# Kernel optimization log

Measured on AMD Instinct MI355X. Metric: run time of the kernel, lower is better.

The kernel has to match this reference:

```python
import jax, jax.numpy as jnp
import numpy as np

EPS = 1e-8

def setup_inputs() -> dict:
    key = jax.random.key(0)
    ks = jax.random.split(key, 7)
    B, S, H, NH, V = 4, 2048, 1024, 8, 2048
    sc = 1.0 / np.sqrt(H)
    return {
        "hidden": jax.random.normal(ks[0], (B, S, H), jnp.float32),
        "prior_w": jax.random.normal(ks[1], (H, NH), jnp.float32) * sc,
        "prior_b": jnp.zeros((NH,), jnp.float32),
        "latent_w": jax.random.normal(ks[2], (H, NH * H), jnp.float32) * sc,
        "latent_b": jnp.zeros((NH * H,), jnp.float32),
        "output_w": jax.random.normal(ks[3], (H, V), jnp.float32) * sc,
        "output_b": jnp.zeros((V,), jnp.float32),
    }

def reference(hidden, prior_w, prior_b, latent_w, latent_b, output_w, output_b):
    B, S, H = hidden.shape
    NH = prior_w.shape[1]
    # prior: sigmoid then renormalize over heads
    prior = jax.nn.sigmoid(hidden @ prior_w + prior_b)              # [B,S,NH]
    prior = prior / (prior.sum(-1, keepdims=True) + EPS)
    # latent: linear -> [B,S,NH,H] -> tanh
    latent = jnp.tanh((hidden @ latent_w + latent_b).reshape(B, S, NH, H))
    # per-head softmax over vocab, weighted sum over heads
    logits = jnp.einsum('bsnh,hv->bsnv', latent, output_w) + output_b
    probs = jax.nn.softmax(logits, axis=-1)                          # [B,S,NH,V]
    return jnp.einsum('bsn,bsnv->bsv', prior, probs)
```

## Files before the change

### kernel.cpp

```cpp
#include <hip/hip_runtime.h>
#include <hip/hip_bf16.h>
#include <stdint.h>

typedef _Float16 f16;
typedef _Float16 f16x8 __attribute__((ext_vector_type(8)));
typedef _Float16 f16x4 __attribute__((ext_vector_type(4)));
typedef float f32x4 __attribute__((ext_vector_type(4)));
typedef float f32x16 __attribute__((ext_vector_type(16)));

#define T_TOK 8192
#define H_DIM 1024
#define NHEAD 8
#define V_DIM 2048

__device__ __forceinline__ void gload16(const void* g, void* l) {
  __builtin_amdgcn_global_load_lds(
      (const __attribute__((address_space(1))) void*)(uintptr_t)g,
      (__attribute__((address_space(3))) void*)(unsigned)(uintptr_t)l,
      16, 0, 0);
}

__device__ __forceinline__ float fast_tanh(float x) {
  float xc = fminf(fmaxf(x, -12.f), 12.f);
  float e = __expf(2.f * xc);
  return (e - 1.f) / (e + 1.f);
}

__device__ __forceinline__ void stage_half(const f16* __restrict__ gRowBase,
                                           char* ldsHalf, int tid, int sl8,
                                           int Kd) {
  const int srow = tid >> 3;
  char* wuni = ldsHalf + ((tid >> 6) << 10);
  gload16(gRowBase + (size_t)srow * Kd + sl8, wuni);
  gload16(gRowBase + (size_t)(srow + 64) * Kd + sl8, wuni + 8192);
}

template <int TANH>
__global__ __launch_bounds__(512, 2) void k_gemm(const f16* __restrict__ A,
                                                 const f16* __restrict__ Bt,
                                                 const float* __restrict__ bias,
                                                 f16* __restrict__ C,
                                                 int M, int N, int K) {
  __shared__ __align__(16) f16 sA[2][16384];
  __shared__ __align__(16) f16 sB[2][16384];
  const int tid = threadIdx.x;
  const int lane = tid & 63;
  const int wid = tid >> 6;
  const int wr = wid >> 2, wc = wid & 3;
  const int gx = gridDim.x;
  const int id = blockIdx.y * gx + blockIdx.x;
  const int cpx = (gx * gridDim.y) >> 3;
  const int sw = (id & 7) * cpx + (id >> 3);
  const int m0 = (sw / gx) * 256, n0 = (sw % gx) * 256;
  const int NT = K >> 6;
  const int sl8 = ((tid & 7) ^ ((tid >> 3) & 7)) << 3;
  const int rr31 = lane & 31;
  const int hi = lane >> 5;
  const int l7 = lane & 7;

  const f16* Ag = A + (size_t)m0 * K;
  const f16* Bg = Bt + (size_t)n0 * K;
  char* sAb = (char*)&sA[0][0];
  char* sBb = (char*)&sB[0][0];

  stage_half(Ag, sAb, tid, sl8, K);
  stage_half(Ag + (size_t)128 * K, sAb + 16384, tid, sl8, K);
  stage_half(Bg, sBb, tid, sl8, K);
  stage_half(Bg + (size_t)128 * K, sBb + 16384, tid, sl8, K);
  stage_half(Bg + 64, sBb + 32768, tid, sl8, K);
  stage_half(Bg + (size_t)128 * K + 64, sBb + 32768 + 16384, tid, sl8, K);
  asm volatile("s_waitcnt vmcnt(4)" ::: "memory");
  __builtin_amdgcn_s_barrier();
  __builtin_amdgcn_sched_barrier(0);

  f32x16 acc[4][2] = {};
  f16x8 af0[4], af1[4], bf[2][4];

#define LDA_SET(dst, base, q)                                                  \
  {                                                                            \
    _Pragma("unroll") for (int mi = 0; mi < 4; ++mi) {                         \
      dst[mi] = *(const f16x8*)((base) + wr * 16384 + mi * 4096 + rr31 * 128 + \
                                (((2 * (q) + hi) ^ l7) << 4));                 \
    }                                                                          \
  }
#define LDB(base)                                                              \
  {                                                                            \
    _Pragma("unroll") for (int n = 0; n < 2; ++n) {                            \
      _Pragma("unroll") for (int ks = 0; ks < 4; ++ks) {                       \
        bf[n][ks] = *(const f16x8*)((base) + wc * 8192 + n * 4096 +            \
                                    rr31 * 128 + (((2 * ks + hi) ^ l7) << 4)); \
      }                                                                        \
    }                                                                          \
  }
#define MFMA8(ks, S)                                                           \
  {                                                                            \
    __builtin_amdgcn_s_setprio(1);                                             \
    _Pragma("unroll") for (int mi = 0; mi < 4; ++mi) {                         \
      _Pragma("unroll") for (int n = 0; n < 2; ++n) {                          \
        acc[mi][n] = __builtin_amdgcn_mfma_f32_32x32x16_f16(                   \
            S[mi], bf[n][ks], acc[mi][n], 0, 0, 0);                            \
      }                                                                        \
    }                                                                          \
    __builtin_amdgcn_s_setprio(0);                                             \
  }

  LDA_SET(af0, sAb, 0);

#define HALF(tt, bc)                                                           \
  {                                                                            \
    const char* cA = sAb + (bc)*32768;                                         \
    const char* cB = sBb + (bc)*32768;                                         \
    char* nA = sAb + ((bc) ^ 1) * 32768;                                       \
    char* nB = sBb + (bc)*32768;                                               \
    const int ktA = ((tt) + 1) << 6, ktB = ((tt) + 2) << 6;                    \
    const bool doA = (tt) + 1 < NT, doB = (tt) + 2 < NT;                       \
                                                                      \
    if (doA) stage_half(Ag + ktA, nA, tid, sl8, K);                            \
    LDB(cB);                                                                   \
    LDA_SET(af1, cA, 1);                                                       \
    __builtin_amdgcn_sched_barrier(0);                                         \
    MFMA8(0, af0);                                                             \
    __builtin_amdgcn_s_barrier();                                              \
                                                                      \
    if (doA) stage_half(Ag + (size_t)128 * K + ktA, nA + 16384, tid, sl8, K);  \
    LDA_SET(af0, cA, 2);                                                       \
    __builtin_amdgcn_sched_barrier(0);                                         \
    MFMA8(1, af1);                                                             \
    __builtin_amdgcn_s_barrier();                                              \
                                                                      \
    if (doB) stage_half(Bg + ktB, nB, tid, sl8, K);                            \
    LDA_SET(af1, cA, 3);                                                       \
    __builtin_amdgcn_sched_barrier(0);                                         \
    MFMA8(2, af0);                                                             \
    __builtin_amdgcn_s_barrier();                                              \
                  \
    if (doB) stage_half(Bg + (size_t)128 * K + ktB, nB + 16384, tid, sl8, K);  \
    if (doB) {                                                                 \
      asm volatile("s_waitcnt vmcnt(4)" ::: "memory");                         \
    } else {                                                                   \
      asm volatile("s_waitcnt vmcnt(0)" ::: "memory");                         \
    }                                                                          \
    __builtin_amdgcn_s_barrier();                                              \
    __builtin_amdgcn_sched_barrier(0);                                         \
    if (doA) LDA_SET(af0, sAb + ((bc) ^ 1) * 32768, 0);                        \
    __builtin_amdgcn_sched_barrier(0);                                         \
    MFMA8(3, af1);                                                             \
  }

#pragma unroll 1
  for (int T = 0; T < NT; T += 2) {
    HALF(T, 0);
    HALF(T + 1, 1);
  }
#undef HALF
#undef LDA_SET
#undef LDB
#undef MFMA8

  const int ccol0 = n0 + wc * 64 + rr31;
  float bv[2];
#pragma unroll
  for (int n = 0; n < 2; ++n) bv[n] = bias[ccol0 + n * 32];
#pragma unroll
  for (int mi = 0; mi < 4; ++mi) {
#pragma unroll
    for (int rq = 0; rq < 4; ++rq) {
#pragma unroll
      for (int r2 = 0; r2 < 4; ++r2) {
        const int row = m0 + wr * 128 + mi * 32 + r2 + 8 * rq + 4 * hi;
        f16* Crow = C + (size_t)row * N;
#pragma unroll
        for (int n = 0; n < 2; ++n) {
          float v = acc[mi][n][rq * 4 + r2] + bv[n];
          if (TANH) v = fast_tanh(v);
          Crow[ccol0 + n * 32] = (f16)v;
        }
      }
    }
  }
}

__global__ __launch_bounds__(256) void k_convert(const float* __restrict__ in,
                                                 f16* __restrict__ out, int n4) {
  int i = blockIdx.x * blockDim.x + threadIdx.x;
  if (i >= n4) return;
  const float4 v = ((const float4*)in)[i];
  f16x4 o;
  o[0] = (f16)v.x; o[1] = (f16)v.y; o[2] = (f16)v.z; o[3] = (f16)v.w;
  ((f16x4*)out)[i] = o;
}

__global__ void k_transpose(const float* __restrict__ in, f16* __restrict__ out,
                            int R, int C) {
  __shared__ f16 tile[32][33];
  int c0 = blockIdx.x * 32, r0 = blockIdx.y * 32;
  for (int j = threadIdx.y; j < 32; j += 8)
    tile[j][threadIdx.x] = (f16)in[(size_t)(r0 + j) * C + (c0 + threadIdx.x)];
  __syncthreads();
  for (int j = threadIdx.y; j < 32; j += 8)
    out[(size_t)(c0 + j) * R + (r0 + threadIdx.x)] = tile[threadIdx.x][j];
}

__global__ __launch_bounds__(256) void k_prior(const float* __restrict__ hidden,
                                               const float* __restrict__ pw,
                                               const float* __restrict__ pb,
                                               float* __restrict__ prior) {
  const int wid = threadIdx.x >> 6, lane = threadIdx.x & 63;
  const int t = blockIdx.x * 4 + wid;
  float acc[NHEAD] = {0.f, 0.f, 0.f, 0.f, 0.f, 0.f, 0.f, 0.f};
  const float* hrow = hidden + (size_t)t * H_DIM;
  for (int k = lane; k < H_DIM; k += 64) {
    float x = hrow[k];
    const float* wr = pw + k * NHEAD;
#pragma unroll
    for (int h = 0; h < NHEAD; ++h) acc[h] += x * wr[h];
  }
#pragma unroll
  for (int h = 0; h < NHEAD; ++h) {
#pragma unroll
    for (int off = 32; off >= 1; off >>= 1) acc[h] += __shfl_xor(acc[h], off);
  }
  if (lane == 0) {
    float p[NHEAD], s = 0.f;
#pragma unroll
    for (int h = 0; h < NHEAD; ++h) {
      p[h] = 1.f / (1.f + __expf(-(acc[h] + pb[h])));
      s += p[h];
    }
    float inv = 1.f / (s + 1e-8f);
#pragma unroll
    for (int h = 0; h < NHEAD; ++h) prior[t * NHEAD + h] = p[h] * inv;
  }
}

__global__ __launch_bounds__(256) void k_softmax(const f16* __restrict__ logits,
                                                 const float* __restrict__ prior,
                                                 float* __restrict__ out) {
  __shared__ float red[4];
  const int t = blockIdx.x;
  const int tid = threadIdx.x, lane = tid & 63, wid = tid >> 6;
  float oa[8] = {0.f, 0.f, 0.f, 0.f, 0.f, 0.f, 0.f, 0.f};
  const int v0 = tid * 8;
#pragma unroll 1
  for (int h = 0; h < NHEAD; ++h) {
    f16x8 x = *(const f16x8*)(logits + ((size_t)t * NHEAD + h) * V_DIM + v0);
    float xv[8], mx = -1e30f;
#pragma unroll
    for (int j = 0; j < 8; j++) { xv[j] = (float)x[j]; mx = fmaxf(mx, xv[j]); }
#pragma unroll
    for (int off = 32; off >= 1; off >>= 1) mx = fmaxf(mx, __shfl_xor(mx, off));
    if (lane == 0) red[wid] = mx;
    __syncthreads();
    mx = fmaxf(fmaxf(red[0], red[1]), fmaxf(red[2], red[3]));
    __syncthreads();
    float e[8], s = 0.f;
#pragma unroll
    for (int j = 0; j < 8; j++) { e[j] = __expf(xv[j] - mx); s += e[j]; }
#pragma unroll
    for (int off = 32; off >= 1; off >>= 1) s += __shfl_xor(s, off);
    if (lane == 0) red[wid] = s;
    __syncthreads();
    s = red[0] + red[1] + red[2] + red[3];
    __syncthreads();
    const float coef = prior[t * NHEAD + h] / s;
#pragma unroll
    for (int j = 0; j < 8; j++) oa[j] += coef * e[j];
  }
  float4* op = (float4*)(out + (size_t)t * V_DIM + v0);
  op[0] = make_float4(oa[0], oa[1], oa[2], oa[3]);
  op[1] = make_float4(oa[4], oa[5], oa[6], oa[7]);
}

extern "C" void kernel_launch(void* const* d_in, const int* in_sizes, int n_in,
                              void* d_out, int out_size, void* d_ws, size_t ws_size,
                              hipStream_t stream) {
  const float* hidden   = (const float*)d_in[0];
  const float* prior_w  = (const float*)d_in[1];
  const float* prior_b  = (const float*)d_in[2];
  const float* latent_w = (const float*)d_in[3];
  const float* latent_b = (const float*)d_in[4];
  const float* output_w = (const float*)d_in[5];
  const float* output_b = (const float*)d_in[6];
  float* out = (float*)d_out;

  char* ws = (char*)d_ws;
  size_t off = 0;
  auto alloc = [&](size_t bytes) -> void* {
    void* p = ws + off;
    off += (bytes + 255) & ~(size_t)255;
    return p;
  };
  f16* hidden_h = (f16*)alloc((size_t)T_TOK * H_DIM * 2);
  f16* lw_t     = (f16*)alloc((size_t)NHEAD * H_DIM * H_DIM * 2);
  f16* ow_t     = (f16*)alloc((size_t)V_DIM * H_DIM * 2);
  float* prior  = (float*)alloc((size_t)T_TOK * NHEAD * 4);

  int tc = T_TOK;
  while (tc > 256) {
    size_t need = off + (size_t)tc * NHEAD * H_DIM * 2 + 256 +
                  (size_t)tc * NHEAD * V_DIM * 2 + 256;
    if (need <= ws_size) break;
    tc >>= 1;
  }
  f16* latent_h = (f16*)alloc((size_t)tc * NHEAD * H_DIM * 2);
  f16* logits_h = (f16*)alloc((size_t)tc * NHEAD * V_DIM * 2);

  k_convert<<<(T_TOK * H_DIM / 4 + 255) / 256, 256, 0, stream>>>(
      hidden, hidden_h, T_TOK * H_DIM / 4);
  k_transpose<<<dim3(NHEAD * H_DIM / 32, H_DIM / 32), dim3(32, 8), 0, stream>>>(
      latent_w, lw_t, H_DIM, NHEAD * H_DIM);
  k_transpose<<<dim3(V_DIM / 32, H_DIM / 32), dim3(32, 8), 0, stream>>>(
      output_w, ow_t, H_DIM, V_DIM);
  k_prior<<<T_TOK / 4, 256, 0, stream>>>(hidden, prior_w, prior_b, prior);

  const int nchunk = T_TOK / tc;
  for (int c = 0; c < nchunk; ++c) {
    const f16* Ah = hidden_h + (size_t)c * tc * H_DIM;
    k_gemm<1><<<dim3(NHEAD * H_DIM / 256, tc / 256), 512, 0, stream>>>(
        Ah, lw_t, latent_b, latent_h, tc, NHEAD * H_DIM, H_DIM);
    k_gemm<0><<<dim3(V_DIM / 256, tc * NHEAD / 256), 512, 0, stream>>>(
        latent_h, ow_t, output_b, logits_h, tc * NHEAD, V_DIM, H_DIM);
    k_softmax<<<tc, 256, 0, stream>>>(logits_h, prior + (size_t)c * tc * NHEAD,
                                      out + (size_t)c * tc * V_DIM);
  }
}
```

Baseline: 600.2 us.

## Stage GEMM tiles through registers with swizzled LDS layout instead of direct-to-LDS loads

Replaces the global_load_lds direct-to-LDS staging with ordinary global loads into registers that are later written to a new XOR-swizzled LDS layout. The K-loop becomes a single-stage-per-iteration double buffer where A and B are both prefetched one tile ahead, replacing the previous asymmetric A/B schedule. B fragments are now loaded per k-substep instead of all at once, which lowers register pressure. It also caps the token chunk size at 2048, giving more chunk launches with smaller intermediates. The cost is extra VGPRs for staging and extra LDS write instructions.

```diff
diff --git a/kernel.cpp b/kernel.cpp
--- a/kernel.cpp
+++ b/kernel.cpp
@@ -13,26 +13,10 @@
 #define NHEAD 8
 #define V_DIM 2048
 
-__device__ __forceinline__ void gload16(const void* g, void* l) {
-  __builtin_amdgcn_global_load_lds(
-      (const __attribute__((address_space(1))) void*)(uintptr_t)g,
-      (__attribute__((address_space(3))) void*)(unsigned)(uintptr_t)l,
-      16, 0, 0);
-}
-
 __device__ __forceinline__ float fast_tanh(float x) {
   float xc = fminf(fmaxf(x, -12.f), 12.f);
   float e = __expf(2.f * xc);
   return (e - 1.f) / (e + 1.f);
-}
-
-__device__ __forceinline__ void stage_half(const f16* __restrict__ gRowBase,
-                                           char* ldsHalf, int tid, int sl8,
-                                           int Kd) {
-  const int srow = tid >> 3;
-  char* wuni = ldsHalf + ((tid >> 6) << 10);
-  gload16(gRowBase + (size_t)srow * Kd + sl8, wuni);
-  gload16(gRowBase + (size_t)(srow + 64) * Kd + sl8, wuni + 8192);
 }
 
 template <int TANH>
@@ -53,108 +37,127 @@
   const int sw = (id & 7) * cpx + (id >> 3);
   const int m0 = (sw / gx) * 256, n0 = (sw % gx) * 256;
   const int NT = K >> 6;
-  const int sl8 = ((tid & 7) ^ ((tid >> 3) & 7)) << 3;
   const int rr31 = lane & 31;
   const int hi = lane >> 5;
-  const int l7 = lane & 7;
-
-  const f16* Ag = A + (size_t)m0 * K;
-  const f16* Bg = Bt + (size_t)n0 * K;
+
+  const int sr = tid >> 3;
+  const int sc = tid & 7;
+  const f16* pA = A + (size_t)(m0 + sr) * K + sc * 8;
+  const f16* pB = Bt + (size_t)(n0 + sr) * K + sc * 8;
+  const size_t rowK = (size_t)64 * K;
   char* sAb = (char*)&sA[0][0];
   char* sBb = (char*)&sB[0][0];
-
-  stage_half(Ag, sAb, tid, sl8, K);
-  stage_half(Ag + (size_t)128 * K, sAb + 16384, tid, sl8, K);
-  stage_half(Bg, sBb, tid, sl8, K);
-  stage_half(Bg + (size_t)128 * K, sBb + 16384, tid, sl8, K);
-  stage_half(Bg + 64, sBb + 32768, tid, sl8, K);
-  stage_half(Bg + (size_t)128 * K + 64, sBb + 32768 + 16384, tid, sl8, K);
-  asm volatile("s_waitcnt vmcnt(4)" ::: "memory");
-  __builtin_amdgcn_s_barrier();
-  __builtin_amdgcn_sched_barrier(0);
+  const int wof = sc * 2048 + ((sr ^ sc) << 4);
 
   f32x16 acc[4][2] = {};
-  f16x8 af0[4], af1[4], bf[2][4];
-
-#define LDA_SET(dst, base, q)                                                  \
-  {                                                                            \
-    _Pragma("unroll") for (int mi = 0; mi < 4; ++mi) {                         \
-      dst[mi] = *(const f16x8*)((base) + wr * 16384 + mi * 4096 + rr31 * 128 + \
-                                (((2 * (q) + hi) ^ l7) << 4));                 \
-    }                                                                          \
-  }
-#define LDB(base)                                                              \
-  {                                                                            \
-    _Pragma("unroll") for (int n = 0; n < 2; ++n) {                            \
-      _Pragma("unroll") for (int ks = 0; ks < 4; ++ks) {                       \
-        bf[n][ks] = *(const f16x8*)((base) + wc * 8192 + n * 4096 +            \
-                                    rr31 * 128 + (((2 * ks + hi) ^ l7) << 4)); \
-      }                                                                        \
-    }                                                                          \
-  }
-#define MFMA8(ks, S)                                                           \
+  f16x8 af0[4], af1[4], bfP[2], bfN[2];
+  f16x8 a0, a1, a2, a3, b0, b1, b2, b3;
+
+#define STAGE_ISSUE(kt)                                                        \
+  {                                                                            \
+    a0 = *(const f16x8*)(pA + (kt));                                           \
+    a1 = *(const f16x8*)(pA + rowK + (kt));                                    \
+    a2 = *(const f16x8*)(pA + 2 * rowK + (kt));                                \
+    a3 = *(const f16x8*)(pA + 3 * rowK + (kt));                                \
+    b0 = *(const f16x8*)(pB + (kt));                                           \
+    b1 = *(const f16x8*)(pB + rowK + (kt));                                    \
+    b2 = *(const f16x8*)(pB + 2 * rowK + (kt));                                \
+    b3 = *(const f16x8*)(pB + 3 * rowK + (kt));                                \
+  }
+#define STAGE_WRITE_A(bb)                                                      \
+  {                                                                            \
+    char* d = sAb + (bb)*32768 + wof;                                          \
+    *(f16x8*)(d) = a0;                                                         \
+    *(f16x8*)(d + 1024) = a1;                                                  \
+    *(f16x8*)(d + 16384) = a2;                                                 \
+    *(f16x8*)(d + 16384 + 1024) = a3;                                          \
+  }
+#define STAGE_WRITE_B(bb)                                                      \
+  {                                                                            \
+    char* d = sBb + (bb)*32768 + wof;                                          \
+    *(f16x8*)(d) = b0;                                                         \
+    *(f16x8*)(d + 1024) = b1;                                                  \
+    *(f16x8*)(d + 16384) = b2;                                                 \
+    *(f16x8*)(d + 16384 + 1024) = b3;                                          \
+  }
+#define LDA4(dst, base, q)                                                     \
+  {                                                                            \
+    const int cq = 2 * (q) + hi;                                               \
+    const char* p = (base) + wr * 16384 + cq * 2048 + ((rr31 ^ cq) << 4);      \
+    dst[0] = *(const f16x8*)(p);                                               \
+    dst[1] = *(const f16x8*)(p + 512);                                         \
+    dst[2] = *(const f16x8*)(p + 1024);                                        \
+    dst[3] = *(const f16x8*)(p + 1536);                                        \
+  }
+#define LDB2(dst, base, q)                                                     \
+  {                                                                            \
+    const int cq = 2 * (q) + hi;                                               \
+    const char* p = (base) + (wc >> 1) * 16384 + cq * 2048 + ((wc & 1) << 10) +\
+                    ((rr31 ^ cq) << 4);                                        \
+    dst[0] = *(const f16x8*)(p);                                               \
+    dst[1] = *(const f16x8*)(p + 512);                                         \
+  }
+#define MFMA8(AF, BF)                                                          \
   {                                                                            \
     __builtin_amdgcn_s_setprio(1);                                             \
     _Pragma("unroll") for (int mi = 0; mi < 4; ++mi) {                         \
       _Pragma("unroll") for (int n = 0; n < 2; ++n) {                          \
         acc[mi][n] = __builtin_amdgcn_mfma_f32_32x32x16_f16(                   \
-            S[mi], bf[n][ks], acc[mi][n], 0, 0, 0);                            \
+            AF[mi], BF[n], acc[mi][n], 0, 0, 0);                               \
       }                                                                        \
     }                                                                          \
     __builtin_amdgcn_s_setprio(0);                                             \
   }
 
-  LDA_SET(af0, sAb, 0);
-
-#define HALF(tt, bc)                                                           \
-  {                                                                            \
-    const char* cA = sAb + (bc)*32768;                                         \
-    const char* cB = sBb + (bc)*32768;                                         \
-    char* nA = sAb + ((bc) ^ 1) * 32768;                                       \
-    char* nB = sBb + (bc)*32768;                                               \
-    const int ktA = ((tt) + 1) << 6, ktB = ((tt) + 2) << 6;                    \
-    const bool doA = (tt) + 1 < NT, doB = (tt) + 2 < NT;                       \
-                                                                      \
-    if (doA) stage_half(Ag + ktA, nA, tid, sl8, K);                            \
-    LDB(cB);                                                                   \
-    LDA_SET(af1, cA, 1);                                                       \
-    __builtin_amdgcn_sched_barrier(0);                                         \
-    MFMA8(0, af0);                                                             \
-    __builtin_amdgcn_s_barrier();                                              \
-                                                                      \
-    if (doA) stage_half(Ag + (size_t)128 * K + ktA, nA + 16384, tid, sl8, K);  \
-    LDA_SET(af0, cA, 2);                                                       \
-    __builtin_amdgcn_sched_barrier(0);                                         \
-    MFMA8(1, af1);                                                             \
-    __builtin_amdgcn_s_barrier();                                              \
-                                                                      \
-    if (doB) stage_half(Bg + ktB, nB, tid, sl8, K);                            \
-    LDA_SET(af1, cA, 3);                                                       \
-    __builtin_amdgcn_sched_barrier(0);                                         \
-    MFMA8(2, af0);                                                             \
-    __builtin_amdgcn_s_barrier();                                              \
-                  \
-    if (doB) stage_half(Bg + (size_t)128 * K + ktB, nB + 16384, tid, sl8, K);  \
-    if (doB) {                                                                 \
-      asm volatile("s_waitcnt vmcnt(4)" ::: "memory");                         \
-    } else {                                                                   \
-      asm volatile("s_waitcnt vmcnt(0)" ::: "memory");                         \
-    }                                                                          \
-    __builtin_amdgcn_s_barrier();                                              \
-    __builtin_amdgcn_sched_barrier(0);                                         \
-    if (doA) LDA_SET(af0, sAb + ((bc) ^ 1) * 32768, 0);                        \
-    __builtin_amdgcn_sched_barrier(0);                                         \
-    MFMA8(3, af1);                                                             \
-  }
-
-#pragma unroll 1
-  for (int T = 0; T < NT; T += 2) {
-    HALF(T, 0);
-    HALF(T + 1, 1);
-  }
-#undef HALF
-#undef LDA_SET
-#undef LDB
+  STAGE_ISSUE(0);
+  STAGE_WRITE_A(0);
+  STAGE_WRITE_B(0);
+  asm volatile("s_waitcnt lgkmcnt(0)" ::: "memory");
+  __builtin_amdgcn_s_barrier();
+  __builtin_amdgcn_sched_barrier(0);
+  LDA4(af0, sAb, 0);
+  LDB2(bfP, sBb, 0);
+
+#pragma unroll 2
+  for (int T = 0; T < NT; ++T) {
+    const int buf = T & 1;
+    const char* cbA = sAb + buf * 32768;
+    const char* cbB = sBb + buf * 32768;
+    const int nb = buf ^ 1;
+    const bool pre = (T + 1 < NT);
+    if (pre) STAGE_ISSUE((size_t)(T + 1) << 6);
+    LDA4(af1, cbA, 1);
+    LDB2(bfN, cbB, 1);
+    __builtin_amdgcn_sched_barrier(0);
+    MFMA8(af0, bfP);
+    __builtin_amdgcn_s_barrier();
+    LDA4(af0, cbA, 2);
+    LDB2(bfP, cbB, 2);
+    __builtin_amdgcn_sched_barrier(0);
+    MFMA8(af1, bfN);
+    __builtin_amdgcn_s_barrier();
+    if (pre) STAGE_WRITE_A(nb);
+    LDA4(af1, cbA, 3);
+    LDB2(bfN, cbB, 3);
+    __builtin_amdgcn_sched_barrier(0);
+    MFMA8(af0, bfP);
+    __builtin_amdgcn_s_barrier();
+    if (pre) STAGE_WRITE_B(nb);
+    asm volatile("s_waitcnt lgkmcnt(0)" ::: "memory");
+    __builtin_amdgcn_s_barrier();
+    __builtin_amdgcn_sched_barrier(0);
+    if (pre) {
+      LDA4(af0, sAb + nb * 32768, 0);
+      LDB2(bfP, sBb + nb * 32768, 0);
+    }
+    __builtin_amdgcn_sched_barrier(0);
+    MFMA8(af1, bfN);
+  }
+#undef STAGE_ISSUE
+#undef STAGE_WRITE_A
+#undef STAGE_WRITE_B
+#undef LDA4
+#undef LDB2
 #undef MFMA8
 
   const int ccol0 = n0 + wc * 64 + rr31;
@@ -295,7 +298,7 @@
   f16* ow_t     = (f16*)alloc((size_t)V_DIM * H_DIM * 2);
   float* prior  = (float*)alloc((size_t)T_TOK * NHEAD * 4);
 
-  int tc = T_TOK;
+  int tc = 2048;
   while (tc > 256) {
     size_t need = off + (size_t)tc * NHEAD * H_DIM * 2 + 256 +
                   (size_t)tc * NHEAD * V_DIM * 2 + 256;
```

New measurement: 622.5 us. 1.04x slower.

## Use N-major tile order for latent GEMM and batch softmax heads

Applied to the files above, without the earlier changes.

Adds a template flag to the GEMM so the latent-projection GEMM walks tiles N-major instead of M-major. This changes which blocks share the same weight columns and aims at better L2 reuse. Separately, the softmax kernel now loads all eight head rows up front and does the max and sum reductions for every head together. That cuts the barriers from 32 to 2 per token and lets the loads overlap. The softmax change raises register use from holding 64 floats per thread.

```diff
diff --git a/kernel.cpp b/kernel.cpp
--- a/kernel.cpp
+++ b/kernel.cpp
@@ -35,7 +35,7 @@
   gload16(gRowBase + (size_t)(srow + 64) * Kd + sl8, wuni + 8192);
 }
 
-template <int TANH>
+template <int TANH, int NMAJ>
 __global__ __launch_bounds__(512, 2) void k_gemm(const f16* __restrict__ A,
                                                  const f16* __restrict__ Bt,
                                                  const float* __restrict__ bias,
@@ -47,11 +47,18 @@
   const int lane = tid & 63;
   const int wid = tid >> 6;
   const int wr = wid >> 2, wc = wid & 3;
-  const int gx = gridDim.x;
+  const int gx = gridDim.x, gy = gridDim.y;
   const int id = blockIdx.y * gx + blockIdx.x;
-  const int cpx = (gx * gridDim.y) >> 3;
+  const int cpx = (gx * gy) >> 3;
   const int sw = (id & 7) * cpx + (id >> 3);
-  const int m0 = (sw / gx) * 256, n0 = (sw % gx) * 256;
+  int m0, n0;
+  if (NMAJ) {
+    n0 = (sw / gy) * 256;
+    m0 = (sw % gy) * 256;
+  } else {
+    m0 = (sw / gx) * 256;
+    n0 = (sw % gx) * 256;
+  }
   const int NT = K >> 6;
   const int sl8 = ((tid & 7) ^ ((tid >> 3) & 7)) << 3;
   const int rr31 = lane & 31;
@@ -236,37 +243,73 @@
 __global__ __launch_bounds__(256) void k_softmax(const f16* __restrict__ logits,
                                                  const float* __restrict__ prior,
                                                  float* __restrict__ out) {
-  __shared__ float red[4];
+  __shared__ float redmx[NHEAD * 4];
+  __shared__ float redsm[NHEAD * 4];
   const int t = blockIdx.x;
   const int tid = threadIdx.x, lane = tid & 63, wid = tid >> 6;
+  const f16* base = logits + (size_t)t * NHEAD * V_DIM + tid * 8;
+
+  f16x8 x[NHEAD];
+#pragma unroll
+  for (int h = 0; h < NHEAD; ++h) x[h] = *(const f16x8*)(base + h * V_DIM);
+
+  float xv[NHEAD][8];
+  float mxl[NHEAD];
+#pragma unroll
+  for (int h = 0; h < NHEAD; ++h) {
+    mxl[h] = -1e30f;
+#pragma unroll
+    for (int j = 0; j < 8; ++j) {
+      xv[h][j] = (float)x[h][j];
+      mxl[h] = fmaxf(mxl[h], xv[h][j]);
+    }
+  }
+#pragma unroll
+  for (int h = 0; h < NHEAD; ++h) {
+#pragma unroll
+    for (int off = 32; off >= 1; off >>= 1)
+      mxl[h] = fmaxf(mxl[h], __shfl_xor(mxl[h], off));
+  }
+  if (lane == 0) {
+#pragma unroll
+    for (int h = 0; h < NHEAD; ++h) redmx[h * 4 + wid] = mxl[h];
+  }
+  __syncthreads();
+
+  float sml[NHEAD];
+#pragma unroll
+  for (int h = 0; h < NHEAD; ++h) {
+    const float mx = fmaxf(fmaxf(redmx[h * 4 + 0], redmx[h * 4 + 1]),
+                           fmaxf(redmx[h * 4 + 2], redmx[h * 4 + 3]));
+    float s = 0.f;
+#pragma unroll
+    for (int j = 0; j < 8; ++j) {
+      xv[h][j] = __expf(xv[h][j] - mx);
+      s += xv[h][j];
+    }
+    sml[h] = s;
+  }
+#pragma unroll
+  for (int h = 0; h < NHEAD; ++h) {
+#pragma unroll
+    for (int off = 32; off >= 1; off >>= 1) sml[h] += __shfl_xor(sml[h], off);
+  }
+  if (lane == 0) {
+#pragma unroll
+    for (int h = 0; h < NHEAD; ++h) redsm[h * 4 + wid] = sml[h];
+  }
+  __syncthreads();
+
   float oa[8] = {0.f, 0.f, 0.f, 0.f, 0.f, 0.f, 0.f, 0.f};
-  const int v0 = tid * 8;
-#pragma unroll 1
-  for (int h = 0; h < NHEAD; ++h) {
-    f16x8 x = *(const f16x8*)(logits + ((size_t)t * NHEAD + h) * V_DIM + v0);
-    float xv[8], mx = -1e30f;
-#pragma unroll
-    for (int j = 0; j < 8; j++) { xv[j] = (float)x[j]; mx = fmaxf(mx, xv[j]); }
-#pragma unroll
-    for (int off = 32; off >= 1; off >>= 1) mx = fmaxf(mx, __shfl_xor(mx, off));
-    if (lane == 0) red[wid] = mx;
-    __syncthreads();
-    mx = fmaxf(fmaxf(red[0], red[1]), fmaxf(red[2], red[3]));
-    __syncthreads();
-    float e[8], s = 0.f;
-#pragma unroll
-    for (int j = 0; j < 8; j++) { e[j] = __expf(xv[j] - mx); s += e[j]; }
-#pragma unroll
-    for (int off = 32; off >= 1; off >>= 1) s += __shfl_xor(s, off);
-    if (lane == 0) red[wid] = s;
-    __syncthreads();
-    s = red[0] + red[1] + red[2] + red[3];
-    __syncthreads();
+#pragma unroll
+  for (int h = 0; h < NHEAD; ++h) {
+    const float s = redsm[h * 4 + 0] + redsm[h * 4 + 1] + redsm[h * 4 + 2] +
+                    redsm[h * 4 + 3];
     const float coef = prior[t * NHEAD + h] / s;
 #pragma unroll
-    for (int j = 0; j < 8; j++) oa[j] += coef * e[j];
-  }
-  float4* op = (float4*)(out + (size_t)t * V_DIM + v0);
+    for (int j = 0; j < 8; ++j) oa[j] += coef * xv[h][j];
+  }
+  float4* op = (float4*)(out + (size_t)t * V_DIM + tid * 8);
   op[0] = make_float4(oa[0], oa[1], oa[2], oa[3]);
   op[1] = make_float4(oa[4], oa[5], oa[6], oa[7]);
 }
@@ -316,9 +359,9 @@
   const int nchunk = T_TOK / tc;
   for (int c = 0; c < nchunk; ++c) {
     const f16* Ah = hidden_h + (size_t)c * tc * H_DIM;
-    k_gemm<1><<<dim3(NHEAD * H_DIM / 256, tc / 256), 512, 0, stream>>>(
+    k_gemm<1, 1><<<dim3(NHEAD * H_DIM / 256, tc / 256), 512, 0, stream>>>(
         Ah, lw_t, latent_b, latent_h, tc, NHEAD * H_DIM, H_DIM);
-    k_gemm<0><<<dim3(V_DIM / 256, tc * NHEAD / 256), 512, 0, stream>>>(
+    k_gemm<0, 0><<<dim3(V_DIM / 256, tc * NHEAD / 256), 512, 0, stream>>>(
         latent_h, ow_t, output_b, logits_h, tc * NHEAD, V_DIM, H_DIM);
     k_softmax<<<tc, 256, 0, stream>>>(logits_h, prior + (size_t)c * tc * NHEAD,
                                       out + (size_t)c * tc * V_DIM);
```

New measurement: 594.7 us. Within noise of the previous version (-0.9%).
